# Kernel tuning notes

Measured on AMD Instinct MI355X. Metric: run time of the kernel, lower is better.

The kernel has to match this reference:

```python
import jax, jax.numpy as jnp
import numpy as np

B, T, D, K = 64, 4096, 90, 32
LOG2PI = 1.8378770664093453


def setup_inputs() -> dict:
    key = jax.random.key(0)
    k1, k2, k3, k4, k5 = jax.random.split(key, 5)
    X = jax.random.normal(k1, (B, T, D), dtype=jnp.float32)
    state_priors = jax.random.uniform(k2, (K,), dtype=jnp.float32)
    transition_matrix = jax.random.uniform(k3, (K, K), dtype=jnp.float32)
    mu = jax.random.normal(k4, (K, D), dtype=jnp.float32) * 0.5
    log_var = jax.random.normal(k5, (K, D), dtype=jnp.float32) * 0.1
    return {"X": X, "state_priors": state_priors,
            "transition_matrix": transition_matrix, "mu": mu, "log_var": log_var}


def _emission_logprobs(X, mu, log_var):
    # Diagonal-Gaussian log density per state: (B,T,K)
    # expand (x-mu)^2*inv_var to avoid materializing a (B,T,K,D) tensor
    inv_var = jnp.exp(-log_var)                                   # (K,D)
    quad = (jnp.einsum('btd,kd->btk', X * X, inv_var)
            - 2.0 * jnp.einsum('btd,kd->btk', X, mu * inv_var)
            + jnp.sum(mu * mu * inv_var, axis=-1))                # (B,T,K)
    return -0.5 * (quad + jnp.sum(log_var, axis=-1) + D * LOG2PI)


def reference(X, state_priors, transition_matrix, mu, log_var):
    log_A = jax.nn.log_softmax(transition_matrix, axis=1)   # (K,K)
    log_pi = jax.nn.log_softmax(state_priors, axis=0)       # (K,)
    em = _emission_logprobs(X, mu, log_var)                 # (B,T,K)

    log_alpha0 = log_pi + em[:, 0, :]                       # (B,K)

    def step(log_alpha, e_t):
        # log_alpha: (B,K), e_t: (B,K)
        la = e_t + jax.nn.logsumexp(log_alpha[:, :, None] + log_A[None], axis=1)
        return la, None

    em_rest = jnp.swapaxes(em[:, 1:, :], 0, 1)              # (T-1,B,K)
    log_alpha_T, _ = jax.lax.scan(step, log_alpha0, em_rest)
    # sum over subjects of logsumexp over states at final timestep
    return jnp.sum(jax.nn.logsumexp(log_alpha_T, axis=-1))
```

## Files before the change

### kernel.cpp

```cpp
#include <hip/hip_runtime.h>
#include <stdint.h>

#define B_ 64
#define T_ 4096
#define D_ 90
#define K_ 32
#define CH_ 32
#define F_  128
#define NB_ 2048

typedef float f32x16 __attribute__((ext_vector_type(16)));
typedef __bf16 bf16x8 __attribute__((ext_vector_type(8)));

#define WS_A     0
#define WS_PI    1024
#define WS_C0    1056
#define WS_WF    1088
#define WS_EACC  4160
#define WS_MS    12352
#define WS_E0    20544
#define WS_Q2    22080

#define LDS_WREG(w) ((w) * 1280)
#define LDS_WF      5120
#define LDS_TOT     11264

__device__ __forceinline__ int perm_r(int r) {
  int t2 = (r >> 2) & 3;
  return r + ((t2 == 1) ? 4 : (t2 == 2) ? -4 : 0);
}
__device__ __forceinline__ uint32_t pk2(float hi, float lo) {
  return __builtin_amdgcn_perm(__float_as_uint(hi), __float_as_uint(lo), 0x07060302u);
}
__device__ __forceinline__ uint32_t rnd_pk(float hi, float lo) {
  uint32_t uh = __float_as_uint(hi) + 0x8000u;
  uint32_t ul = __float_as_uint(lo) + 0x8000u;
  return __builtin_amdgcn_perm(uh, ul, 0x07060302u);
}
__device__ __forceinline__ float bf2f(ushort u) {
  return __uint_as_float(((uint32_t)u) << 16);
}
__device__ __forceinline__ bf16x8 mkbf(uint32_t a, uint32_t b, uint32_t c, uint32_t d) {
  union { uint32_t u[4]; bf16x8 v; } x;
  x.u[0] = a; x.u[1] = b; x.u[2] = c; x.u[3] = d;
  return x.v;
}

__global__ __launch_bounds__(1024) void prep_kernel(
    const float* __restrict__ priors, const float* __restrict__ trans,
    const float* __restrict__ mu, const float* __restrict__ lv,
    float* __restrict__ ws) {
  int tid = threadIdx.x;
  {
    float v = trans[tid];
    float m = v;
    #pragma unroll
    for (int mk = 16; mk; mk >>= 1) m = fmaxf(m, __shfl_xor(m, mk));
    float e = expf(v - m);
    float s = e;
    #pragma unroll
    for (int mk = 16; mk; mk >>= 1) s += __shfl_xor(s, mk);
    ws[WS_A + tid] = e / s;
  }
  if (tid < 32) {
    float v = priors[tid];
    float m = v;
    #pragma unroll
    for (int mk = 16; mk; mk >>= 1) m = fmaxf(m, __shfl_xor(m, mk));
    float e = expf(v - m);
    float s = e;
    #pragma unroll
    for (int mk = 16; mk; mk >>= 1) s += __shfl_xor(s, mk);
    ws[WS_PI + tid] = e / s;
  }
  for (int i = tid; i < 6144; i += 1024) {
    int j = i & 7, l = (i >> 3) & 63, cm = i >> 9;
    int c = cm >> 1, mat = cm & 1;
    int h = l >> 5, nn = l & 31;
    int d = 16 * c + 8 * h + j;
    float v = 0.0f;
    if (d < D_) {
      float ivd = expf(-lv[nn * D_ + d]);
      v = (mat == 0) ? -0.5f * ivd : mu[nn * D_ + d] * ivd;
    }
    ((ushort*)(ws + WS_WF))[i] = (ushort)((__float_as_uint(v) + 0x8000u) >> 16);
  }
  if (tid < 32) {
    float s = 0.0f;
    for (int d = 0; d < D_; ++d) {
      float l  = lv[tid * D_ + d];
      float iv = expf(-l);
      float m_ = mu[tid * D_ + d];
      s += m_ * m_ * iv + l;
    }
    ws[WS_C0 + tid] = -0.5f * (s + (float)D_ * 1.8378770664093453f);
  }
}

__global__ __launch_bounds__(256, 6) void fused_kernel(const float* __restrict__ X,
                                                       float* __restrict__ ws,
                                                       float* __restrict__ out) {
  __shared__ __align__(16) ushort sh[LDS_TOT];
  __shared__ float msb[4];
  __shared__ int   peb[4];
  int tid = threadIdx.x;
  int l = tid & 63, w = tid >> 6;
  int n = l & 31, h = l >> 5;
  int tB = blockIdx.x << 7;
  int t0 = tB + (w << 5);
  int b  = t0 >> 12;
  if (blockIdx.x == 0 && tid == 0) *out = 0.0f;

  {
    const uint4* wfp = (const uint4*)((const ushort*)(ws + WS_WF));
    uint4* wfl = (uint4*)(sh + LDS_WF);
    #pragma unroll
    for (int k = 0; k < 3; ++k) wfl[tid + (k << 8)] = wfp[tid + (k << 8)];
  }
  float c0 = ws[WS_C0 + n];

  int srow = l >> 1, sp = l & 1;
  const float* xg = X + (size_t)(t0 + srow) * D_ + 8 * sp;
  ushort* xbuf = sh + LDS_WREG(w);
  float2 va[4];
  auto xload = [&](int c) {
    #pragma unroll
    for (int s = 0; s < 4; ++s) {
      int d = 16 * c + 8 * sp + 2 * s;
      if (d < D_) va[s] = *(const float2*)(xg + 16 * c + 2 * s);
      else { va[s].x = 0.0f; va[s].y = 0.0f; }
    }
  };
  auto xwrite = [&]() {
    uint4 pkv;
    pkv.x = rnd_pk(va[0].y, va[0].x);
    pkv.y = rnd_pk(va[1].y, va[1].x);
    pkv.z = rnd_pk(va[2].y, va[2].x);
    pkv.w = rnd_pk(va[3].y, va[3].x);
    *(uint4*)(xbuf + srow * 24 + 8 * sp) = pkv;
  };
  xload(0);
  xwrite();
  xload(1);
  __syncthreads();

  const ushort* wfl = sh + LDS_WF;
  f32x16 acc;
  #pragma unroll
  for (int r = 0; r < 16; ++r) acc[r] = 0.0f;
  #pragma unroll
  for (int c = 0; c < 6; ++c) {
    union { uint4 u; bf16x8 v; } xb;
    xb.u = *(const uint4*)(xbuf + n * 24 + 8 * h);
    float x[8];
    #pragma unroll
    for (int j = 0; j < 8; ++j) {
      uint32_t uu = ((const uint32_t*)&xb.u)[j >> 1];
      x[j] = bf2f((j & 1) ? (ushort)(uu >> 16) : (ushort)(uu & 0xFFFF));
    }
    union { uint32_t u[4]; bf16x8 v; } x2b;
    #pragma unroll
    for (int r = 0; r < 4; ++r)
      x2b.u[r] = rnd_pk(x[2*r+1] * x[2*r+1], x[2*r] * x[2*r]);
    union { uint4 u; bf16x8 v; } w1, w2;
    w2.u = *(const uint4*)(wfl + (2 * c)     * 512 + l * 8);
    w1.u = *(const uint4*)(wfl + (2 * c + 1) * 512 + l * 8);
    acc = __builtin_amdgcn_mfma_f32_32x32x16_bf16(xb.v,  w1.v, acc, 0, 0, 0);
    acc = __builtin_amdgcn_mfma_f32_32x32x16_bf16(x2b.v, w2.v, acc, 0, 0, 0);
    if (c < 5) {
      xwrite();
      if (c < 4) xload(c + 2);
    }
  }
  float em[16], mrow[16];
  #pragma unroll
  for (int r = 0; r < 16; ++r) {
    float v = acc[r] + c0;
    em[r] = v;
    float m = v;
    #pragma unroll
    for (int mk = 1; mk <= 16; mk <<= 1) m = fmaxf(m, __shfl_xor(m, mk));
    mrow[r] = m;
  }
  ushort* Ew = sh + LDS_WREG(w);
  #pragma unroll
  for (int q = 0; q < 4; ++q) {
    float e0 = exp2f((em[4*q]   - mrow[4*q])   * 1.44269504088896f);
    float e1 = exp2f((em[4*q+1] - mrow[4*q+1]) * 1.44269504088896f);
    float e2 = exp2f((em[4*q+2] - mrow[4*q+2]) * 1.44269504088896f);
    float e3 = exp2f((em[4*q+3] - mrow[4*q+3]) * 1.44269504088896f);
    uint2 d;
    d.x = rnd_pk(e1, e0);
    d.y = rnd_pk(e3, e2);
    *(uint2*)(Ew + n * 40 + 8 * q + 4 * h) = d;
    if (q == 0 && h == 0 && (t0 & (T_ - 1)) == 0)
      ((ushort*)(ws + WS_E0))[b * K_ + n] = (ushort)(d.x & 0xFFFF);
  }
  float msum = 0.0f;
  #pragma unroll
  for (int r = 0; r < 16; ++r) msum += mrow[r];
  msum += __shfl_xor(msum, 32);
  if (l == 0) msb[w] = msum;

  int col = perm_r(n);
  const float* A = ws + WS_A;
  float astat[16];
  #pragma unroll
  for (int j = 0; j < 8; ++j) {
    astat[j]     = A[(8 * h + j) * K_ + col];
    astat[8 + j] = A[(16 + 8 * h + j) * K_ + col];
  }
  uint32_t q[8];
  #pragma unroll
  for (int r = 0; r < 4; ++r) {
    int s0 = 8 * h + 2 * r;
    uint32_t lo = (s0 == n)     ? 0x3F80u : 0u;
    uint32_t hi = (s0 + 1 == n) ? 0x3F80u : 0u;
    q[r] = lo | (hi << 16);
    int s2 = s0 + 16;
    lo = (s2 == n)     ? 0x3F80u : 0u;
    hi = (s2 + 1 == n) ? 0x3F80u : 0u;
    q[4 + r] = lo | (hi << 16);
  }
  int eacc = 0;
  const f32x16 z = {0.f,0.f,0.f,0.f,0.f,0.f,0.f,0.f,0.f,0.f,0.f,0.f,0.f,0.f,0.f,0.f};
  #pragma unroll
  for (int r = 0; r < 16; ++r) acc[r] = 0.0f;

  auto step = [&](float e0) {
    uint32_t au[8];
    #pragma unroll
    for (int r = 0; r < 4; ++r) {
      au[r]     = pk2(astat[2 * r + 1] * e0, astat[2 * r] * e0);
      au[4 + r] = pk2(astat[8 + 2 * r + 1] * e0, astat[8 + 2 * r] * e0);
    }
    bf16x8 alo = mkbf(au[0], au[1], au[2], au[3]);
    bf16x8 ahi = mkbf(au[4], au[5], au[6], au[7]);
    bf16x8 qlo = mkbf(q[0], q[1], q[2], q[3]);
    bf16x8 qhi = mkbf(q[4], q[5], q[6], q[7]);
    acc = __builtin_amdgcn_mfma_f32_32x32x16_bf16(alo, qlo, z, 0, 0, 0);
    acc = __builtin_amdgcn_mfma_f32_32x32x16_bf16(ahi, qhi, acc, 0, 0, 0);
    #pragma unroll
    for (int r = 0; r < 4; ++r) {
      q[r]     = pk2(acc[2 * r + 1], acc[2 * r]);
      q[4 + r] = pk2(acc[8 + 2 * r + 1], acc[8 + 2 * r]);
    }
  };
  auto lmul = [&](uint4 lo, uint4 hi) {
    bf16x8 alo = mkbf(lo.x, lo.y, lo.z, lo.w);
    bf16x8 ahi = mkbf(hi.x, hi.y, hi.z, hi.w);
    bf16x8 qlo = mkbf(q[0], q[1], q[2], q[3]);
    bf16x8 qhi = mkbf(q[4], q[5], q[6], q[7]);
    acc = __builtin_amdgcn_mfma_f32_32x32x16_bf16(alo, qlo, z, 0, 0, 0);
    acc = __builtin_amdgcn_mfma_f32_32x32x16_bf16(ahi, qhi, acc, 0, 0, 0);
    #pragma unroll
    for (int r = 0; r < 4; ++r) {
      q[r]     = pk2(acc[2 * r + 1], acc[2 * r]);
      q[4 + r] = pk2(acc[8 + 2 * r + 1], acc[8 + 2 * r]);
    }
  };
  auto renorm = [&]() {
    float m = acc[0];
    #pragma unroll
    for (int r = 1; r < 16; ++r) m = fmaxf(m, acc[r]);
    #pragma unroll
    for (int mk = 1; mk <= 32; mk <<= 1) m = fmaxf(m, __shfl_xor(m, mk));
    int ex;
    frexpf(m, &ex);
    float sc = ldexpf(1.0f, -ex);
    eacc += ex;
    #pragma unroll
    for (int r = 0; r < 16; ++r) acc[r] *= sc;
    #pragma unroll
    for (int r = 0; r < 4; ++r) {
      q[r]     = pk2(acc[2 * r + 1], acc[2 * r]);
      q[4 + r] = pk2(acc[8 + 2 * r + 1], acc[8 + 2 * r]);
    }
  };

  const ushort* Eb = sh + LDS_WREG(w) + col * 40;
  int g0 = 0;
  if ((t0 & (T_ - 1)) == 0) {
    uint4 ev = *(const uint4*)(Eb);
    #pragma unroll
    for (int j = 1; j < 8; ++j) {
      uint32_t u = ((const uint32_t*)&ev)[j >> 1];
      step(bf2f((j & 1) ? (ushort)(u >> 16) : (ushort)(u & 0xFFFF)));
    }
    renorm();
    g0 = 1;
  }
  for (int g = g0; g < CH_ / 8; ++g) {
    uint4 ev = *(const uint4*)(Eb + 8 * g);
    #pragma unroll
    for (int j = 0; j < 8; ++j) {
      uint32_t u = ((const uint32_t*)&ev)[j >> 1];
      step(bf2f((j & 1) ? (ushort)(u >> 16) : (ushort)(u & 0xFFFF)));
    }
    renorm();
  }

  ushort* Qw = sh + LDS_WREG(w);
  #pragma unroll
  for (int r = 0; r < 16; ++r) {
    int m_ = (r & 3) + 8 * (r >> 2) + 4 * h;
    Qw[perm_r(m_) * 40 + n] = (ushort)(__float_as_uint(acc[r]) >> 16);
  }
  if (l == 0) peb[w] = eacc;
  __syncthreads();
  if (w != 0) return;

  #pragma unroll
  for (int r = 0; r < 4; ++r) {
    int s0 = 8 * h + 2 * r;
    uint32_t lo = (s0 == n)     ? 0x3F80u : 0u;
    uint32_t hi = (s0 + 1 == n) ? 0x3F80u : 0u;
    q[r] = lo | (hi << 16);
    int s2 = s0 + 16;
    lo = (s2 == n)     ? 0x3F80u : 0u;
    hi = (s2 + 1 == n) ? 0x3F80u : 0u;
    q[4 + r] = lo | (hi << 16);
  }
  eacc = peb[0] + peb[1] + peb[2] + peb[3];
  float msm = msb[0] + msb[1] + msb[2] + msb[3];
  #pragma unroll
  for (int p = 0; p < 4; ++p) {
    const ushort* base = sh + LDS_WREG(p) + col * 40;
    uint4 lo = *(const uint4*)(base + 8 * h);
    uint4 hi = *(const uint4*)(base + 16 + 8 * h);
    lmul(lo, hi);
  }
  renorm();
  ushort* Qo = (ushort*)(ws + WS_Q2) + (size_t)blockIdx.x * (K_ * K_);
  #pragma unroll
  for (int r = 0; r < 16; ++r) {
    int m_ = (r & 3) + 8 * (r >> 2) + 4 * h;
    Qo[perm_r(m_) * K_ + n] = (ushort)(__float_as_uint(acc[r]) >> 16);
  }
  if (l == 0) {
    ((int*)ws)[WS_EACC + blockIdx.x] = eacc;
    ws[WS_MS + blockIdx.x] = msm;
  }
}

__global__ __launch_bounds__(256) void combine_kernel(float* __restrict__ ws,
                                                      float* __restrict__ out) {
  __shared__ __align__(16) ushort pm[4][1280];
  __shared__ int pe[4];
  int tid = threadIdx.x;
  int l = tid & 63, w = tid >> 6;
  int h = l >> 5, n = l & 31;
  int b = blockIdx.x;
  int row = perm_r(n);
  int eacc;
  {
    const int* ea = ((const int*)ws) + WS_EACC + b * 32 + w * 8;
    int v = (l < 8) ? ea[l] : 0;
    #pragma unroll
    for (int mk = 1; mk <= 4; mk <<= 1) v += __shfl_xor(v, mk);
    eacc = __shfl(v, 0);
  }
  uint32_t q[8];
  #pragma unroll
  for (int r = 0; r < 4; ++r) {
    int s0 = 8 * h + 2 * r;
    uint32_t lo = (s0 == n)     ? 0x3F80u : 0u;
    uint32_t hi = (s0 + 1 == n) ? 0x3F80u : 0u;
    q[r] = lo | (hi << 16);
    int s2 = s0 + 16;
    lo = (s2 == n)     ? 0x3F80u : 0u;
    hi = (s2 + 1 == n) ? 0x3F80u : 0u;
    q[4 + r] = lo | (hi << 16);
  }
  f32x16 acc;
  #pragma unroll
  for (int r = 0; r < 16; ++r) acc[r] = 0.0f;
  const f32x16 z = {0.f,0.f,0.f,0.f,0.f,0.f,0.f,0.f,0.f,0.f,0.f,0.f,0.f,0.f,0.f,0.f};

  auto lmul = [&](uint4 lo, uint4 hi) {
    bf16x8 alo = mkbf(lo.x, lo.y, lo.z, lo.w);
    bf16x8 ahi = mkbf(hi.x, hi.y, hi.z, hi.w);
    bf16x8 qlo = mkbf(q[0], q[1], q[2], q[3]);
    bf16x8 qhi = mkbf(q[4], q[5], q[6], q[7]);
    acc = __builtin_amdgcn_mfma_f32_32x32x16_bf16(alo, qlo, z, 0, 0, 0);
    acc = __builtin_amdgcn_mfma_f32_32x32x16_bf16(ahi, qhi, acc, 0, 0, 0);
    #pragma unroll
    for (int r = 0; r < 4; ++r) {
      q[r]     = pk2(acc[2 * r + 1], acc[2 * r]);
      q[4 + r] = pk2(acc[8 + 2 * r + 1], acc[8 + 2 * r]);
    }
  };
  auto renorm = [&]() {
    float m = acc[0];
    #pragma unroll
    for (int r = 1; r < 16; ++r) m = fmaxf(m, acc[r]);
    #pragma unroll
    for (int mk = 1; mk <= 32; mk <<= 1) m = fmaxf(m, __shfl_xor(m, mk));
    int ex;
    frexpf(m, &ex);
    float sc = ldexpf(1.0f, -ex);
    eacc += ex;
    #pragma unroll
    for (int r = 0; r < 16; ++r) acc[r] *= sc;
    #pragma unroll
    for (int r = 0; r < 4; ++r) {
      q[r]     = pk2(acc[2 * r + 1], acc[2 * r]);
      q[4 + r] = pk2(acc[8 + 2 * r + 1], acc[8 + 2 * r]);
    }
  };

  const ushort* Qb = (const ushort*)(ws + WS_Q2) + (size_t)(b * 32 + w * 8) * (K_ * K_);
  #pragma unroll
  for (int p = 0; p < 8; ++p) {
    const ushort* Mc = Qb + (size_t)p * (K_ * K_) + row * K_;
    uint4 lo = *(const uint4*)(Mc + 8 * h);
    uint4 hi = *(const uint4*)(Mc + 16 + 8 * h);
    lmul(lo, hi);
    if ((p & 3) == 3) renorm();
  }
  #pragma unroll
  for (int r = 0; r < 16; ++r) {
    int m_ = (r & 3) + 8 * (r >> 2) + 4 * h;
    pm[w][perm_r(m_) * 40 + n] = (ushort)(__float_as_uint(acc[r]) >> 16);
  }
  if (l == 0) pe[w] = eacc;
  __syncthreads();
  if (w != 0) return;

  float alpha0 = ws[WS_PI + n] * bf2f(((const ushort*)(ws + WS_E0))[b * K_ + n]);
  float msm;
  {
    float v = (l < 32) ? ws[WS_MS + b * 32 + l] : 0.0f;
    #pragma unroll
    for (int mk = 1; mk <= 32; mk <<= 1) v += __shfl_xor(v, mk);
    msm = v;
  }
  #pragma unroll
  for (int r = 0; r < 4; ++r) {
    int s0 = 8 * h + 2 * r;
    uint32_t lo = (s0 == n)     ? 0x3F80u : 0u;
    uint32_t hi = (s0 + 1 == n) ? 0x3F80u : 0u;
    q[r] = lo | (hi << 16);
    int s2 = s0 + 16;
    lo = (s2 == n)     ? 0x3F80u : 0u;
    hi = (s2 + 1 == n) ? 0x3F80u : 0u;
    q[4 + r] = lo | (hi << 16);
  }
  #pragma unroll
  for (int r = 0; r < 16; ++r) acc[r] = 0.0f;
  int et = pe[0] + pe[1] + pe[2] + pe[3];
  #pragma unroll
  for (int p = 0; p < 4; ++p) {
    const ushort* base = pm[p] + row * 40;
    uint4 lo = *(const uint4*)(base + 8 * h);
    uint4 hi = *(const uint4*)(base + 16 + 8 * h);
    lmul(lo, hi);
  }
  float part = 0.0f;
  #pragma unroll
  for (int r = 0; r < 16; ++r) part += acc[r];
  part *= alpha0;
  #pragma unroll
  for (int mk = 1; mk <= 32; mk <<= 1) part += __shfl_xor(part, mk);
  if (l == 0) {
    float res = logf(part) + (float)et * 0.69314718055994531f + msm;
    atomicAdd(out, res);
  }
}

extern "C" void kernel_launch(void* const* d_in, const int* in_sizes, int n_in,
                              void* d_out, int out_size, void* d_ws, size_t ws_size,
                              hipStream_t stream) {
  (void)in_sizes; (void)n_in; (void)out_size; (void)ws_size;
  const float* X      = (const float*)d_in[0];
  const float* priors = (const float*)d_in[1];
  const float* trans  = (const float*)d_in[2];
  const float* mu     = (const float*)d_in[3];
  const float* lv     = (const float*)d_in[4];
  float* ws  = (float*)d_ws;
  float* out = (float*)d_out;
  prep_kernel<<<1, 1024, 0, stream>>>(priors, trans, mu, lv, ws);
  fused_kernel<<<NB_, 256, 0, stream>>>(X, ws, out);
  combine_kernel<<<B_, 256, 0, stream>>>(ws, out);
}
```

Measured before the change: 174.6 us.

## Give each wave two interleaved 32-step chunks to hide MFMA dependency latency

Each block now covers 256 timesteps, and each wave handles two 32-step chunks. The two chunks' transfer-matrix products run as independent chains that alternate, so their MFMA latencies overlap and fill stalls in the serial recurrence. The block-level composition now multiplies 8 chunk matrices, and the grid shrinks to 1024 blocks, which halves the work in the combine kernel. In exchange LDS use and register pressure go up and launch bounds occupancy drops from 6 to 4 blocks per CU. A stray label also appears in the code.

```diff
diff --git a/kernel.cpp b/kernel.cpp
--- a/kernel.cpp
+++ b/kernel.cpp
@@ -6,8 +6,7 @@
 #define D_ 90
 #define K_ 32
 #define CH_ 32
-#define F_  128
-#define NB_ 2048
+#define NB_ 1024
 
 typedef float f32x16 __attribute__((ext_vector_type(16)));
 typedef __bf16 bf16x8 __attribute__((ext_vector_type(8)));
@@ -21,9 +20,9 @@
 #define WS_E0    20544
 #define WS_Q2    22080
 
-#define LDS_WREG(w) ((w) * 1280)
-#define LDS_WF      5120
-#define LDS_TOT     11264
+#define LDS_CREG(c) ((c) * 1280)
+#define LDS_WF      10240
+#define LDS_TOT     16384
 
 __device__ __forceinline__ int perm_r(int r) {
   int t2 = (r >> 2) & 3;
@@ -97,7 +96,7 @@
   }
 }
 
-__global__ __launch_bounds__(256, 6) void fused_kernel(const float* __restrict__ X,
+__global__ __launch_bounds__(256, 4) void fused_kernel(const float* __restrict__ X,
                                                        float* __restrict__ ws,
                                                        float* __restrict__ out) {
   __shared__ __align__(16) ushort sh[LDS_TOT];
@@ -106,8 +105,8 @@
   int tid = threadIdx.x;
   int l = tid & 63, w = tid >> 6;
   int n = l & 31, h = l >> 5;
-  int tB = blockIdx.x << 7;
-  int t0 = tB + (w << 5);
+  int tB = blockIdx.x << 8;
+  int t0 = tB + (w << 6);
   int b  = t0 >> 12;
   if (blockIdx.x == 0 && tid == 0) *out = 0.0f;
 
@@ -120,10 +119,9 @@
   float c0 = ws[WS_C0 + n];
 
   int srow = l >> 1, sp = l & 1;
-  const float* xg = X + (size_t)(t0 + srow) * D_ + 8 * sp;
-  ushort* xbuf = sh + LDS_WREG(w);
+  const float* xg0 = X + (size_t)(t0 + srow) * D_ + 8 * sp;
   float2 va[4];
-  auto xload = [&](int c) {
+  auto xload = [&](const float* xg, int c) {
     #pragma unroll
     for (int s = 0; s < 4; ++s) {
       int d = 16 * c + 8 * sp + 2 * s;
@@ -131,74 +129,80 @@
       else { va[s].x = 0.0f; va[s].y = 0.0f; }
     }
   };
-  auto xwrite = [&]() {
+  auto xwrite = [&](ushort* xb) {
     uint4 pkv;
     pkv.x = rnd_pk(va[0].y, va[0].x);
     pkv.y = rnd_pk(va[1].y, va[1].x);
     pkv.z = rnd_pk(va[2].y, va[2].x);
     pkv.w = rnd_pk(va[3].y, va[3].x);
-    *(uint4*)(xbuf + srow * 24 + 8 * sp) = pkv;
-  };
-  xload(0);
-  xwrite();
-  xload(1);
+    *(uint4*)(xb + srow * 24 + 8 * sp) = pkv;
+  };
+  xload(xg0, 0);
+  xwrite(sh + LDS_CREG(2 * w));
+  xload(xg0, 1);
   __syncthreads();
 
   const ushort* wfl = sh + LDS_WF;
-  f32x16 acc;
-  #pragma unroll
-  for (int r = 0; r < 16; ++r) acc[r] = 0.0f;
-  #pragma unroll
-  for (int c = 0; c < 6; ++c) {
-    union { uint4 u; bf16x8 v; } xb;
-    xb.u = *(const uint4*)(xbuf + n * 24 + 8 * h);
-    float x[8];
-    #pragma unroll
-    for (int j = 0; j < 8; ++j) {
-      uint32_t uu = ((const uint32_t*)&xb.u)[j >> 1];
-      x[j] = bf2f((j & 1) ? (ushort)(uu >> 16) : (ushort)(uu & 0xFFFF));
-    }
-    union { uint32_t u[4]; bf16x8 v; } x2b;
-    #pragma unroll
-    for (int r = 0; r < 4; ++r)
-      x2b.u[r] = rnd_pk(x[2*r+1] * x[2*r+1], x[2*r] * x[2*r]);
-    union { uint4 u; bf16x8 v; } w1, w2;
-    w2.u = *(const uint4*)(wfl + (2 * c)     * 512 + l * 8);
-    w1.u = *(const uint4*)(wfl + (2 * c + 1) * 512 + l * 8);
-    acc = __builtin_amdgcn_mfma_f32_32x32x16_bf16(xb.v,  w1.v, acc, 0, 0, 0);
-    acc = __builtin_amdgcn_mfma_f32_32x32x16_bf16(x2b.v, w2.v, acc, 0, 0, 0);
-    if (c < 5) {
-      xwrite();
-      if (c < 4) xload(c + 2);
-    }
-  }
-  float em[16], mrow[16];
-  #pragma unroll
-  for (int r = 0; r < 16; ++r) {
-    float v = acc[r] + c0;
-    em[r] = v;
-    float m = v;
-    #pragma unroll
-    for (int mk = 1; mk <= 16; mk <<= 1) m = fmaxf(m, __shfl_xor(m, mk));
-    mrow[r] = m;
-  }
-  ushort* Ew = sh + LDS_WREG(w);
-  #pragma unroll
-  for (int q = 0; q < 4; ++q) {
-    float e0 = exp2f((em[4*q]   - mrow[4*q])   * 1.44269504088896f);
-    float e1 = exp2f((em[4*q+1] - mrow[4*q+1]) * 1.44269504088896f);
-    float e2 = exp2f((em[4*q+2] - mrow[4*q+2]) * 1.44269504088896f);
-    float e3 = exp2f((em[4*q+3] - mrow[4*q+3]) * 1.44269504088896f);
-    uint2 d;
-    d.x = rnd_pk(e1, e0);
-    d.y = rnd_pk(e3, e2);
-    *(uint2*)(Ew + n * 40 + 8 * q + 4 * h) = d;
-    if (q == 0 && h == 0 && (t0 & (T_ - 1)) == 0)
-      ((ushort*)(ws + WS_E0))[b * K_ + n] = (ushort)(d.x & 0xFFFF);
-  }
+  bool firstA = ((t0 & (T_ - 1)) == 0);
   float msum = 0.0f;
   #pragma unroll
-  for (int r = 0; r < 16; ++r) msum += mrow[r];
+  for (int i = 0; i < 2; ++i) {
+    const float* xg = xg0 + (size_t)(32 * i) * D_;
+    ushort* xbuf = sh + LDS_CREG(2 * w + i);
+    if (i == 1) { xload(xg, 0); xwrite(xbuf); xload(xg, 1); }
+    f32x16 acc;
+    #pragma unroll
+    for (int r = 0; r < 16; ++r) acc[r] = 0.0f;
+    #pragma unroll
+    for (int c = 0; c < 6; ++c) {
+      union { uint4 u; bf16x8 v; } xb;
+      xb.u = *(const uint4*)(xbuf + n * 24 + 8 * h);
+      float x[8];
+      #pragma unroll
+      for (int j = 0; j < 8; ++j) {
+        uint32_t uu = ((const uint32_t*)&xb.u)[j >> 1];
+        x[j] = bf2f((j & 1) ? (ushort)(uu >> 16) : (ushort)(uu & 0xFFFF));
+      }
+      union { uint32_t u[4]; bf16x8 v; } x2b;
+      #pragma unroll
+      for (int r = 0; r < 4; ++r)
+        x2b.u[r] = rnd_pk(x[2*r+1] * x[2*r+1], x[2*r] * x[2*r]);
+      union { uint4 u; bf16x8 v; } w1, w2;
+      w2.u = *(const uint4*)(wfl + (2 * c)     * 512 + l * 8);
+      w1.u = *(const uint4*)(wfl + (2 * c + 1) * 512 + l * 8);
+      acc = __builtin_amdgcn_mfma_f32_32x32x16_bf16(xb.v,  w1.v, acc, 0, 0, 0);
+      acc = __builtin_amdgcn_mfma_f32_32x32x16_bf16(x2b.v, w2.v, acc, 0, 0, 0);
+      if (c < 5) {
+        xwrite(xbuf);
+        if (c < 4) xload(xg, c + 2);
+      }
+    }
+    float em[16], mrow[16];
+    #pragma unroll
+    for (int r = 0; r < 16; ++r) {
+      float v = acc[r] + c0;
+      em[r] = v;
+      float m = v;
+      #pragma unroll
+      for (int mk = 1; mk <= 16; mk <<= 1) m = fmaxf(m, __shfl_xor(m, mk));
+      mrow[r] = m;
+    }
+    #pragma unroll
+    for (int q = 0; q < 4; ++q) {
+      float e0 = exp2f((em[4*q]   - mrow[4*q])   * 1.44269504088896f);
+      float e1 = exp2f((em[4*q+1] - mrow[4*q+1]) * 1.44269504088896f);
+      float e2 = exp2f((em[4*q+2] - mrow[4*q+2]) * 1.44269504088896f);
+      float e3 = exp2f((em[4*q+3] - mrow[4*q+3]) * 1.44269504088896f);
+      uint2 d;
+      d.x = rnd_pk(e1, e0);
+      d.y = rnd_pk(e3, e2);
+      *(uint2*)(xbuf + n * 40 + 8 * q + 4 * h) = d;
+      if (i == 0 && q == 0 && h == 0 && firstA)
+        ((ushort*)(ws + WS_E0))[b * K_ + n] = (ushort)(d.x & 0xFFFF);
+    }
+    #pragma unroll
+    for (int r = 0; r < 16; ++r) msum += mrow[r];
+  }
   msum += __shfl_xor(msum, 32);
   if (l == 0) msb[w] = msum;
 
@@ -210,24 +214,25 @@
     astat[j]     = A[(8 * h + j) * K_ + col];
     astat[8 + j] = A[(16 + 8 * h + j) * K_ + col];
   }
-  uint32_t q[8];
+  int eacc = 0;
+  const f32x16 z = {0.f,0.f,0.f,0.f,0.f,0.f,0.f,0.f,0.f,0.f,0.f,0.f,0.f,0.f,0.f,0.f};
+  f32x16 accA, accB;
+  uint32_t qA[8], qB[8];
+  #pragma unroll
+  for (int r = 0; r < 16; ++r) { accA[r] = 0.0f; accB[r] = 0.0f; }
   #pragma unroll
   for (int r = 0; r < 4; ++r) {
     int s0 = 8 * h + 2 * r;
     uint32_t lo = (s0 == n)     ? 0x3F80u : 0u;
     uint32_t hi = (s0 + 1 == n) ? 0x3F80u : 0u;
-    q[r] = lo | (hi << 16);
+    qA[r] = lo | (hi << 16);  qB[r] = qA[r];
     int s2 = s0 + 16;
     lo = (s2 == n)     ? 0x3F80u : 0u;
     hi = (s2 + 1 == n) ? 0x3F80u : 0u;
-    q[4 + r] = lo | (hi << 16);
-  }
-  int eacc = 0;
-  const f32x16 z = {0.f,0.f,0.f,0.f,0.f,0.f,0.f,0.f,0.f,0.f,0.f,0.f,0.f,0.f,0.f,0.f};
-  #pragma unroll
-  for (int r = 0; r < 16; ++r) acc[r] = 0.0f;
-
-  auto step = [&](float e0) {
+    qA[4 + r] = lo | (hi << 16);  qB[4 + r] = qA[4 + r];
+  }
+
+  auto stepc = [&](f32x16& acc, uint32_t (&q)[8], float e0) {
     uint32_t au[8];
     #pragma unroll
     for (int r = 0; r < 4; ++r) {
@@ -246,20 +251,7 @@
       q[4 + r] = pk2(acc[8 + 2 * r + 1], acc[8 + 2 * r]);
     }
   };
-  auto lmul = [&](uint4 lo, uint4 hi) {
-    bf16x8 alo = mkbf(lo.x, lo.y, lo.z, lo.w);
-    bf16x8 ahi = mkbf(hi.x, hi.y, hi.z, hi.w);
-    bf16x8 qlo = mkbf(q[0], q[1], q[2], q[3]);
-    bf16x8 qhi = mkbf(q[4], q[5], q[6], q[7]);
-    acc = __builtin_amdgcn_mfma_f32_32x32x16_bf16(alo, qlo, z, 0, 0, 0);
-    acc = __builtin_amdgcn_mfma_f32_32x32x16_bf16(ahi, qhi, acc, 0, 0, 0);
-    #pragma unroll
-    for (int r = 0; r < 4; ++r) {
-      q[r]     = pk2(acc[2 * r + 1], acc[2 * r]);
-      q[4 + r] = pk2(acc[8 + 2 * r + 1], acc[8 + 2 * r]);
-    }
-  };
-  auto renorm = [&]() {
+  auto renormc = [&](f32x16& acc, uint32_t (&q)[8]) {
     float m = acc[0];
     #pragma unroll
     for (int r = 1; r < 16; ++r) m = fmaxf(m, acc[r]);
@@ -278,33 +270,34 @@
     }
   };
 
-  const ushort* Eb = sh + LDS_WREG(w) + col * 40;
-  int g0 = 0;
-  if ((t0 & (T_ - 1)) == 0) {
-    uint4 ev = *(const uint4*)(Eb);
-    #pragma unroll
-    for (int j = 1; j < 8; ++j) {
-      uint32_t u = ((const uint32_t*)&ev)[j >> 1];
-      step(bf2f((j & 1) ? (ushort)(u >> 16) : (ushort)(u & 0xFFFF)));
-    }
-    renorm();
-    g0 = 1;
-  }
-  for (int g = g0; g < CH_ / 8; ++g) {
-    uint4 ev = *(const uint4*)(Eb + 8 * g);
+  const ushort* EbA = sh + LDS_CREG(2 * w)     + col * 40;
+  const ushort* EbB = sh + LDS_CREG(2 * w + 1) + col * 40;
+  #pragma unroll
+  for (int g = 0; g < 4; ++g) {
+    uint4 evA = *(const uint4*)(EbA + 8 * g);
+    uint4 evB = *(const uint4*)(EbB + 8 * g);
     #pragma unroll
     for (int j = 0; j < 8; ++j) {
-      uint32_t u = ((const uint32_t*)&ev)[j >> 1];
-      step(bf2f((j & 1) ? (ushort)(u >> 16) : (ushort)(u & 0xFFFF)));
-    }
-    renorm();
-  }
-
-  ushort* Qw = sh + LDS_WREG(w);
+      uint32_t uA = ((const uint32_t*)&evA)[j >> 1];
+      uint32_t uB = ((const uint32_t*)&evB)[j >> 1];
+      float eA = bf2f((j & 1) ? (ushort)(uA >> 16) : (ushort)(uA & 0xFFFF));
+      float eB = bf2f((j & 1) ? (ushort)(uB >> 16) : (ushort)(uB & 0xFFFF));
+      if (g == 0 && j == 0) {
+        if (!firstA) stepc(accA, qA, eA);
+      } else {
+        stepc(accA, qA, eA);
+      }
+      stepc(accB, qB, eB);
+    }
+    renormc(accA, qA);
+    renormc(accB, qB);
+  }
+
   #pragma unroll
   for (int r = 0; r < 16; ++r) {
-    int m_ = (r & 3) + 8 * (r >> 2) + 4 * h;
-    Qw[perm_r(m_) * 40 + n] = (ushort)(__float_as_uint(acc[r]) >> 16);
+    int m_ = perm_r((r & 3) + 8 * (r >> 2) + 4 * h) * 40 + n;
+    (sh + LDS_CREG(2 * w))[m_]     = (ushort)(__float_as_uint(accA[r]) >> 16);
+    (sh + LDS_CREG(2 * w + 1))[m_] = (ushort)(__float_as_uint(accB[r]) >> 16);
   }
   if (l == 0) peb[w] = eacc;
   __syncthreads();
@@ -315,27 +308,41 @@
     int s0 = 8 * h + 2 * r;
     uint32_t lo = (s0 == n)     ? 0x3F80u : 0u;
     uint32_t hi = (s0 + 1 == n) ? 0x3F80u : 0u;
-    q[r] = lo | (hi << 16);
+    qA[r] = lo | (hi << 16);
     int s2 = s0 + 16;
     lo = (s2 == n)     ? 0x3F80u : 0u;
     hi = (s2 + 1 == n) ? 0x3F80u : 0u;
-    q[4 + r] = lo | (hi << 16);
+    qA[4 + r] = lo | (hi << 16);
   }
   eacc = peb[0] + peb[1] + peb[2] + peb[3];
   float msm = msb[0] + msb[1] + msb[2] + msb[3];
   #pragma unroll
-  for (int p = 0; p < 4; ++p) {
-    const ushort* base = sh + LDS_WREG(p) + col * 40;
+  for (int r = 0; r < 16; ++r) accA[r] = 0.0f;
+  #pragma unroll
+  for (int p = 0; p < 8; ++p) {
+    const ushort* base = sh + LDS_CREG(p) + col * 40;
     uint4 lo = *(const uint4*)(base + 8 * h);
     uint4 hi = *(const uint4*)(base + 16 + 8 * h);
-    lmul(lo, hi);
-  }
-  renorm();
+    stepcompose:;
+    bf16x8 alo = mkbf(lo.x, lo.y, lo.z, lo.w);
+    bf16x8 ahi = mkbf(hi.x, hi.y, hi.z, hi.w);
+    bf16x8 qlo = mkbf(qA[0], qA[1], qA[2], qA[3]);
+    bf16x8 qhi = mkbf(qA[4], qA[5], qA[6], qA[7]);
+    accA = __builtin_amdgcn_mfma_f32_32x32x16_bf16(alo, qlo, z, 0, 0, 0);
+    accA = __builtin_amdgcn_mfma_f32_32x32x16_bf16(ahi, qhi, accA, 0, 0, 0);
+    #pragma unroll
+    for (int r = 0; r < 4; ++r) {
+      qA[r]     = pk2(accA[2 * r + 1], accA[2 * r]);
+      qA[4 + r] = pk2(accA[8 + 2 * r + 1], accA[8 + 2 * r]);
+    }
+    if (p == 3) renormc(accA, qA);
+  }
+  renormc(accA, qA);
   ushort* Qo = (ushort*)(ws + WS_Q2) + (size_t)blockIdx.x * (K_ * K_);
   #pragma unroll
   for (int r = 0; r < 16; ++r) {
     int m_ = (r & 3) + 8 * (r >> 2) + 4 * h;
-    Qo[perm_r(m_) * K_ + n] = (ushort)(__float_as_uint(acc[r]) >> 16);
+    Qo[perm_r(m_) * K_ + n] = (ushort)(__float_as_uint(accA[r]) >> 16);
   }
   if (l == 0) {
     ((int*)ws)[WS_EACC + blockIdx.x] = eacc;
@@ -354,10 +361,10 @@
   int row = perm_r(n);
   int eacc;
   {
-    const int* ea = ((const int*)ws) + WS_EACC + b * 32 + w * 8;
-    int v = (l < 8) ? ea[l] : 0;
-    #pragma unroll
-    for (int mk = 1; mk <= 4; mk <<= 1) v += __shfl_xor(v, mk);
+    const int* ea = ((const int*)ws) + WS_EACC + b * 16 + w * 4;
+    int v = (l < 4) ? ea[l] : 0;
+    #pragma unroll
+    for (int mk = 1; mk <= 2; mk <<= 1) v += __shfl_xor(v, mk);
     eacc = __shfl(v, 0);
   }
   uint32_t q[8];
@@ -409,15 +416,15 @@
     }
   };
 
-  const ushort* Qb = (const ushort*)(ws + WS_Q2) + (size_t)(b * 32 + w * 8) * (K_ * K_);
-  #pragma unroll
-  for (int p = 0; p < 8; ++p) {
+  const ushort* Qb = (const ushort*)(ws + WS_Q2) + (size_t)(b * 16 + w * 4) * (K_ * K_);
+  #pragma unroll
+  for (int p = 0; p < 4; ++p) {
     const ushort* Mc = Qb + (size_t)p * (K_ * K_) + row * K_;
     uint4 lo = *(const uint4*)(Mc + 8 * h);
     uint4 hi = *(const uint4*)(Mc + 16 + 8 * h);
     lmul(lo, hi);
-    if ((p & 3) == 3) renorm();
-  }
+  }
+  renorm();
   #pragma unroll
   for (int r = 0; r < 16; ++r) {
     int m_ = (r & 3) + 8 * (r >> 2) + 4 * h;
@@ -430,7 +437,7 @@
   float alpha0 = ws[WS_PI + n] * bf2f(((const ushort*)(ws + WS_E0))[b * K_ + n]);
   float msm;
   {
-    float v = (l < 32) ? ws[WS_MS + b * 32 + l] : 0.0f;
+    float v = (l < 16) ? ws[WS_MS + b * 16 + l] : 0.0f;
     #pragma unroll
     for (int mk = 1; mk <= 32; mk <<= 1) v += __shfl_xor(v, mk);
     msm = v;
```

After: 183.8 us. 1.05x slower.

## Move per-block chunk matrix reduction from fused kernel into combine kernel

Applied to the files above, without the earlier changes.

Each wave in the fused kernel now writes its own 32-step transfer matrix, exponent and max-sum straight to global workspace. The old intra-block barrier, where wave 0 multiplied four matrices while the others sat idle, is gone. The combine kernel now chains 32 matrices per wave instead of 8, with a 4-deep register prefetch of the global loads and a renormalisation every 8 products. LDS padding shrinks and the launch bound rises to 8 blocks per CU to allow higher occupancy. The trade-off is more global traffic and a longer serial MFMA chain in the combine kernel.

```diff
diff --git a/kernel.cpp b/kernel.cpp
--- a/kernel.cpp
+++ b/kernel.cpp
@@ -19,11 +19,11 @@
 #define WS_EACC  4160
 #define WS_MS    12352
 #define WS_E0    20544
-#define WS_Q2    22080
-
-#define LDS_WREG(w) ((w) * 1280)
-#define LDS_WF      5120
-#define LDS_TOT     11264
+#define WS_Q     22080
+
+#define LDS_WREG(w) ((w) * 1024)
+#define LDS_WF      4096
+#define LDS_TOT     10240
 
 __device__ __forceinline__ int perm_r(int r) {
   int t2 = (r >> 2) & 3;
@@ -97,18 +97,17 @@
   }
 }
 
-__global__ __launch_bounds__(256, 6) void fused_kernel(const float* __restrict__ X,
+__global__ __launch_bounds__(256, 8) void fused_kernel(const float* __restrict__ X,
                                                        float* __restrict__ ws,
                                                        float* __restrict__ out) {
   __shared__ __align__(16) ushort sh[LDS_TOT];
-  __shared__ float msb[4];
-  __shared__ int   peb[4];
   int tid = threadIdx.x;
   int l = tid & 63, w = tid >> 6;
   int n = l & 31, h = l >> 5;
   int tB = blockIdx.x << 7;
   int t0 = tB + (w << 5);
   int b  = t0 >> 12;
+  int bc = t0 >> 5;
   if (blockIdx.x == 0 && tid == 0) *out = 0.0f;
 
   {
@@ -172,35 +171,30 @@
       if (c < 4) xload(c + 2);
     }
   }
-  float em[16], mrow[16];
-  #pragma unroll
-  for (int r = 0; r < 16; ++r) {
-    float v = acc[r] + c0;
-    em[r] = v;
-    float m = v;
-    #pragma unroll
-    for (int mk = 1; mk <= 16; mk <<= 1) m = fmaxf(m, __shfl_xor(m, mk));
-    mrow[r] = m;
-  }
-  ushort* Ew = sh + LDS_WREG(w);
-  #pragma unroll
-  for (int q = 0; q < 4; ++q) {
-    float e0 = exp2f((em[4*q]   - mrow[4*q])   * 1.44269504088896f);
-    float e1 = exp2f((em[4*q+1] - mrow[4*q+1]) * 1.44269504088896f);
-    float e2 = exp2f((em[4*q+2] - mrow[4*q+2]) * 1.44269504088896f);
-    float e3 = exp2f((em[4*q+3] - mrow[4*q+3]) * 1.44269504088896f);
+  bool first = ((t0 & (T_ - 1)) == 0);
+  ushort* Ew = xbuf;
+  float msum = 0.0f;
+  #pragma unroll
+  for (int qq = 0; qq < 4; ++qq) {
+    float e0[4];
+    #pragma unroll
+    for (int i = 0; i < 4; ++i) {
+      float v = acc[4 * qq + i] + c0;
+      float m = v;
+      #pragma unroll
+      for (int mk = 1; mk <= 16; mk <<= 1) m = fmaxf(m, __shfl_xor(m, mk));
+      e0[i] = exp2f((v - m) * 1.44269504088896f);
+      msum += m;
+    }
     uint2 d;
-    d.x = rnd_pk(e1, e0);
-    d.y = rnd_pk(e3, e2);
-    *(uint2*)(Ew + n * 40 + 8 * q + 4 * h) = d;
-    if (q == 0 && h == 0 && (t0 & (T_ - 1)) == 0)
+    d.x = rnd_pk(e0[1], e0[0]);
+    d.y = rnd_pk(e0[3], e0[2]);
+    *(uint2*)(Ew + n * 32 + 8 * qq + 4 * h) = d;
+    if (qq == 0 && h == 0 && first)
       ((ushort*)(ws + WS_E0))[b * K_ + n] = (ushort)(d.x & 0xFFFF);
   }
-  float msum = 0.0f;
-  #pragma unroll
-  for (int r = 0; r < 16; ++r) msum += mrow[r];
   msum += __shfl_xor(msum, 32);
-  if (l == 0) msb[w] = msum;
+  if (l == 0) ws[WS_MS + bc] = msum;
 
   int col = perm_r(n);
   const float* A = ws + WS_A;
@@ -246,19 +240,6 @@
       q[4 + r] = pk2(acc[8 + 2 * r + 1], acc[8 + 2 * r]);
     }
   };
-  auto lmul = [&](uint4 lo, uint4 hi) {
-    bf16x8 alo = mkbf(lo.x, lo.y, lo.z, lo.w);
-    bf16x8 ahi = mkbf(hi.x, hi.y, hi.z, hi.w);
-    bf16x8 qlo = mkbf(q[0], q[1], q[2], q[3]);
-    bf16x8 qhi = mkbf(q[4], q[5], q[6], q[7]);
-    acc = __builtin_amdgcn_mfma_f32_32x32x16_bf16(alo, qlo, z, 0, 0, 0);
-    acc = __builtin_amdgcn_mfma_f32_32x32x16_bf16(ahi, qhi, acc, 0, 0, 0);
-    #pragma unroll
-    for (int r = 0; r < 4; ++r) {
-      q[r]     = pk2(acc[2 * r + 1], acc[2 * r]);
-      q[4 + r] = pk2(acc[8 + 2 * r + 1], acc[8 + 2 * r]);
-    }
-  };
   auto renorm = [&]() {
     float m = acc[0];
     #pragma unroll
@@ -278,9 +259,9 @@
     }
   };
 
-  const ushort* Eb = sh + LDS_WREG(w) + col * 40;
+  const ushort* Eb = sh + LDS_WREG(w) + col * 32;
   int g0 = 0;
-  if ((t0 & (T_ - 1)) == 0) {
+  if (first) {
     uint4 ev = *(const uint4*)(Eb);
     #pragma unroll
     for (int j = 1; j < 8; ++j) {
@@ -300,47 +281,13 @@
     renorm();
   }
 
-  ushort* Qw = sh + LDS_WREG(w);
-  #pragma unroll
-  for (int r = 0; r < 16; ++r) {
-    int m_ = (r & 3) + 8 * (r >> 2) + 4 * h;
-    Qw[perm_r(m_) * 40 + n] = (ushort)(__float_as_uint(acc[r]) >> 16);
-  }
-  if (l == 0) peb[w] = eacc;
-  __syncthreads();
-  if (w != 0) return;
-
-  #pragma unroll
-  for (int r = 0; r < 4; ++r) {
-    int s0 = 8 * h + 2 * r;
-    uint32_t lo = (s0 == n)     ? 0x3F80u : 0u;
-    uint32_t hi = (s0 + 1 == n) ? 0x3F80u : 0u;
-    q[r] = lo | (hi << 16);
-    int s2 = s0 + 16;
-    lo = (s2 == n)     ? 0x3F80u : 0u;
-    hi = (s2 + 1 == n) ? 0x3F80u : 0u;
-    q[4 + r] = lo | (hi << 16);
-  }
-  eacc = peb[0] + peb[1] + peb[2] + peb[3];
-  float msm = msb[0] + msb[1] + msb[2] + msb[3];
-  #pragma unroll
-  for (int p = 0; p < 4; ++p) {
-    const ushort* base = sh + LDS_WREG(p) + col * 40;
-    uint4 lo = *(const uint4*)(base + 8 * h);
-    uint4 hi = *(const uint4*)(base + 16 + 8 * h);
-    lmul(lo, hi);
-  }
-  renorm();
-  ushort* Qo = (ushort*)(ws + WS_Q2) + (size_t)blockIdx.x * (K_ * K_);
+  ushort* Qo = (ushort*)(ws + WS_Q) + (size_t)bc * (K_ * K_);
   #pragma unroll
   for (int r = 0; r < 16; ++r) {
     int m_ = (r & 3) + 8 * (r >> 2) + 4 * h;
     Qo[perm_r(m_) * K_ + n] = (ushort)(__float_as_uint(acc[r]) >> 16);
   }
-  if (l == 0) {
-    ((int*)ws)[WS_EACC + blockIdx.x] = eacc;
-    ws[WS_MS + blockIdx.x] = msm;
-  }
+  if (l == 0) ((int*)ws)[WS_EACC + bc] = eacc;
 }
 
 __global__ __launch_bounds__(256) void combine_kernel(float* __restrict__ ws,
@@ -354,10 +301,10 @@
   int row = perm_r(n);
   int eacc;
   {
-    const int* ea = ((const int*)ws) + WS_EACC + b * 32 + w * 8;
-    int v = (l < 8) ? ea[l] : 0;
-    #pragma unroll
-    for (int mk = 1; mk <= 4; mk <<= 1) v += __shfl_xor(v, mk);
+    const int* ea = ((const int*)ws) + WS_EACC + b * F_ + w * 32;
+    int v = (l < 32) ? ea[l] : 0;
+    #pragma unroll
+    for (int mk = 1; mk <= 16; mk <<= 1) v += __shfl_xor(v, mk);
     eacc = __shfl(v, 0);
   }
   uint32_t q[8];
@@ -409,14 +356,23 @@
     }
   };
 
-  const ushort* Qb = (const ushort*)(ws + WS_Q2) + (size_t)(b * 32 + w * 8) * (K_ * K_);
-  #pragma unroll
-  for (int p = 0; p < 8; ++p) {
+  const ushort* Qb = (const ushort*)(ws + WS_Q) + (size_t)(b * F_ + w * 32) * (K_ * K_);
+  uint4 rlo[4], rhi[4];
+  #pragma unroll
+  for (int p = 0; p < 4; ++p) {
     const ushort* Mc = Qb + (size_t)p * (K_ * K_) + row * K_;
-    uint4 lo = *(const uint4*)(Mc + 8 * h);
-    uint4 hi = *(const uint4*)(Mc + 16 + 8 * h);
-    lmul(lo, hi);
-    if ((p & 3) == 3) renorm();
+    rlo[p] = *(const uint4*)(Mc + 8 * h);
+    rhi[p] = *(const uint4*)(Mc + 16 + 8 * h);
+  }
+  #pragma unroll
+  for (int c = 0; c < 32; ++c) {
+    lmul(rlo[c & 3], rhi[c & 3]);
+    if (c + 4 < 32) {
+      const ushort* Mc = Qb + (size_t)(c + 4) * (K_ * K_) + row * K_;
+      rlo[c & 3] = *(const uint4*)(Mc + 8 * h);
+      rhi[c & 3] = *(const uint4*)(Mc + 16 + 8 * h);
+    }
+    if ((c & 7) == 7) renorm();
   }
   #pragma unroll
   for (int r = 0; r < 16; ++r) {
@@ -430,7 +386,7 @@
   float alpha0 = ws[WS_PI + n] * bf2f(((const ushort*)(ws + WS_E0))[b * K_ + n]);
   float msm;
   {
-    float v = (l < 32) ? ws[WS_MS + b * 32 + l] : 0.0f;
+    float v = ws[WS_MS + b * F_ + l] + ws[WS_MS + b * F_ + 64 + l];
     #pragma unroll
     for (int mk = 1; mk <= 32; mk <<= 1) v += __shfl_xor(v, mk);
     msm = v;
```

After: 182.0 us. 4.3% more time.

## Double fused-kernel block size to 8 waves, halving blocks and combine partials

Applied to the files above, without the earlier changes.

Each block of the fused kernel now has 8 waves covering 256 timesteps instead of 4 waves covering 128. Each block therefore reduces 8 chunk matrices in-block, and the combine kernel has only 16 partial products per sequence to multiply instead of 32. The emission softmax epilogue is restructured to reuse the X staging buffer and use fewer live registers, and the C0 prep is parallelised across 1024 threads with a shuffle reduction. The larger blocks reduce global partial traffic and combine work, but make the serial in-block product chain longer and may lower occupancy under the new launch bounds.

```diff
diff --git a/kernel.cpp b/kernel.cpp
--- a/kernel.cpp
+++ b/kernel.cpp
@@ -6,8 +6,7 @@
 #define D_ 90
 #define K_ 32
 #define CH_ 32
-#define F_  128
-#define NB_ 2048
+#define NB_ 1024
 
 typedef float f32x16 __attribute__((ext_vector_type(16)));
 typedef __bf16 bf16x8 __attribute__((ext_vector_type(8)));
@@ -22,8 +21,8 @@
 #define WS_Q2    22080
 
 #define LDS_WREG(w) ((w) * 1280)
-#define LDS_WF      5120
-#define LDS_TOT     11264
+#define LDS_WF      10240
+#define LDS_TOT     16384
 
 __device__ __forceinline__ int perm_r(int r) {
   int t2 = (r >> 2) & 3;
@@ -85,28 +84,31 @@
     }
     ((ushort*)(ws + WS_WF))[i] = (ushort)((__float_as_uint(v) + 0x8000u) >> 16);
   }
-  if (tid < 32) {
+  {
+    int nn = tid >> 5, j = tid & 31;
     float s = 0.0f;
-    for (int d = 0; d < D_; ++d) {
-      float l  = lv[tid * D_ + d];
-      float iv = expf(-l);
-      float m_ = mu[tid * D_ + d];
-      s += m_ * m_ * iv + l;
-    }
-    ws[WS_C0 + tid] = -0.5f * (s + (float)D_ * 1.8378770664093453f);
-  }
-}
-
-__global__ __launch_bounds__(256, 6) void fused_kernel(const float* __restrict__ X,
+    for (int d = j; d < D_; d += 32) {
+      float lvv = lv[nn * D_ + d];
+      float iv  = expf(-lvv);
+      float m_  = mu[nn * D_ + d];
+      s += m_ * m_ * iv + lvv;
+    }
+    #pragma unroll
+    for (int mk = 16; mk; mk >>= 1) s += __shfl_xor(s, mk);
+    if (j == 0) ws[WS_C0 + nn] = -0.5f * (s + (float)D_ * 1.8378770664093453f);
+  }
+}
+
+__global__ __launch_bounds__(512, 8) void fused_kernel(const float* __restrict__ X,
                                                        float* __restrict__ ws,
                                                        float* __restrict__ out) {
   __shared__ __align__(16) ushort sh[LDS_TOT];
-  __shared__ float msb[4];
-  __shared__ int   peb[4];
+  __shared__ float msb[8];
+  __shared__ int   peb[8];
   int tid = threadIdx.x;
   int l = tid & 63, w = tid >> 6;
   int n = l & 31, h = l >> 5;
-  int tB = blockIdx.x << 7;
+  int tB = blockIdx.x << 8;
   int t0 = tB + (w << 5);
   int b  = t0 >> 12;
   if (blockIdx.x == 0 && tid == 0) *out = 0.0f;
@@ -115,7 +117,10 @@
     const uint4* wfp = (const uint4*)((const ushort*)(ws + WS_WF));
     uint4* wfl = (uint4*)(sh + LDS_WF);
     #pragma unroll
-    for (int k = 0; k < 3; ++k) wfl[tid + (k << 8)] = wfp[tid + (k << 8)];
+    for (int k = 0; k < 2; ++k) {
+      int i = tid + (k << 9);
+      if (i < 768) wfl[i] = wfp[i];
+    }
   }
   float c0 = ws[WS_C0 + n];
 
@@ -172,33 +177,27 @@
       if (c < 4) xload(c + 2);
     }
   }
-  float em[16], mrow[16];
-  #pragma unroll
-  for (int r = 0; r < 16; ++r) {
-    float v = acc[r] + c0;
-    em[r] = v;
-    float m = v;
-    #pragma unroll
-    for (int mk = 1; mk <= 16; mk <<= 1) m = fmaxf(m, __shfl_xor(m, mk));
-    mrow[r] = m;
-  }
-  ushort* Ew = sh + LDS_WREG(w);
-  #pragma unroll
-  for (int q = 0; q < 4; ++q) {
-    float e0 = exp2f((em[4*q]   - mrow[4*q])   * 1.44269504088896f);
-    float e1 = exp2f((em[4*q+1] - mrow[4*q+1]) * 1.44269504088896f);
-    float e2 = exp2f((em[4*q+2] - mrow[4*q+2]) * 1.44269504088896f);
-    float e3 = exp2f((em[4*q+3] - mrow[4*q+3]) * 1.44269504088896f);
+  bool first = ((t0 & (T_ - 1)) == 0);
+  float msum = 0.0f;
+  #pragma unroll
+  for (int qq = 0; qq < 4; ++qq) {
+    float e0[4];
+    #pragma unroll
+    for (int i = 0; i < 4; ++i) {
+      float v = acc[4 * qq + i] + c0;
+      float m = v;
+      #pragma unroll
+      for (int mk = 1; mk <= 16; mk <<= 1) m = fmaxf(m, __shfl_xor(m, mk));
+      e0[i] = exp2f((v - m) * 1.44269504088896f);
+      msum += m;
+    }
     uint2 d;
-    d.x = rnd_pk(e1, e0);
-    d.y = rnd_pk(e3, e2);
-    *(uint2*)(Ew + n * 40 + 8 * q + 4 * h) = d;
-    if (q == 0 && h == 0 && (t0 & (T_ - 1)) == 0)
+    d.x = rnd_pk(e0[1], e0[0]);
+    d.y = rnd_pk(e0[3], e0[2]);
+    *(uint2*)(xbuf + n * 40 + 8 * qq + 4 * h) = d;
+    if (qq == 0 && h == 0 && first)
       ((ushort*)(ws + WS_E0))[b * K_ + n] = (ushort)(d.x & 0xFFFF);
   }
-  float msum = 0.0f;
-  #pragma unroll
-  for (int r = 0; r < 16; ++r) msum += mrow[r];
   msum += __shfl_xor(msum, 32);
   if (l == 0) msb[w] = msum;
 
@@ -280,7 +279,7 @@
 
   const ushort* Eb = sh + LDS_WREG(w) + col * 40;
   int g0 = 0;
-  if ((t0 & (T_ - 1)) == 0) {
+  if (first) {
     uint4 ev = *(const uint4*)(Eb);
     #pragma unroll
     for (int j = 1; j < 8; ++j) {
@@ -321,14 +320,19 @@
     hi = (s2 + 1 == n) ? 0x3F80u : 0u;
     q[4 + r] = lo | (hi << 16);
   }
-  eacc = peb[0] + peb[1] + peb[2] + peb[3];
-  float msm = msb[0] + msb[1] + msb[2] + msb[3];
-  #pragma unroll
-  for (int p = 0; p < 4; ++p) {
+  eacc = 0;
+  float msm = 0.0f;
+  #pragma unroll
+  for (int p = 0; p < 8; ++p) { eacc += peb[p]; msm += msb[p]; }
+  #pragma unroll
+  for (int r = 0; r < 16; ++r) acc[r] = 0.0f;
+  #pragma unroll
+  for (int p = 0; p < 8; ++p) {
     const ushort* base = sh + LDS_WREG(p) + col * 40;
     uint4 lo = *(const uint4*)(base + 8 * h);
     uint4 hi = *(const uint4*)(base + 16 + 8 * h);
     lmul(lo, hi);
+    if (p == 3) renorm();
   }
   renorm();
   ushort* Qo = (ushort*)(ws + WS_Q2) + (size_t)blockIdx.x * (K_ * K_);
@@ -354,10 +358,10 @@
   int row = perm_r(n);
   int eacc;
   {
-    const int* ea = ((const int*)ws) + WS_EACC + b * 32 + w * 8;
-    int v = (l < 8) ? ea[l] : 0;
-    #pragma unroll
-    for (int mk = 1; mk <= 4; mk <<= 1) v += __shfl_xor(v, mk);
+    const int* ea = ((const int*)ws) + WS_EACC + b * 16 + w * 4;
+    int v = (l < 4) ? ea[l] : 0;
+    #pragma unroll
+    for (int mk = 1; mk <= 2; mk <<= 1) v += __shfl_xor(v, mk);
     eacc = __shfl(v, 0);
   }
   uint32_t q[8];
@@ -409,15 +413,15 @@
     }
   };
 
-  const ushort* Qb = (const ushort*)(ws + WS_Q2) + (size_t)(b * 32 + w * 8) * (K_ * K_);
-  #pragma unroll
-  for (int p = 0; p < 8; ++p) {
+  const ushort* Qb = (const ushort*)(ws + WS_Q2) + (size_t)(b * 16 + w * 4) * (K_ * K_);
+  #pragma unroll
+  for (int p = 0; p < 4; ++p) {
     const ushort* Mc = Qb + (size_t)p * (K_ * K_) + row * K_;
     uint4 lo = *(const uint4*)(Mc + 8 * h);
     uint4 hi = *(const uint4*)(Mc + 16 + 8 * h);
     lmul(lo, hi);
-    if ((p & 3) == 3) renorm();
-  }
+  }
+  renorm();
   #pragma unroll
   for (int r = 0; r < 16; ++r) {
     int m_ = (r & 3) + 8 * (r >> 2) + 4 * h;
@@ -430,7 +434,7 @@
   float alpha0 = ws[WS_PI + n] * bf2f(((const ushort*)(ws + WS_E0))[b * K_ + n]);
   float msm;
   {
-    float v = (l < 32) ? ws[WS_MS + b * 32 + l] : 0.0f;
+    float v = (l < 16) ? ws[WS_MS + b * 16 + l] : 0.0f;
     #pragma unroll
     for (int mk = 1; mk <= 32; mk <<= 1) v += __shfl_xor(v, mk);
     msm = v;
@@ -480,6 +484,6 @@
   float* ws  = (float*)d_ws;
   float* out = (float*)d_out;
   prep_kernel<<<1, 1024, 0, stream>>>(priors, trans, mu, lv, ws);
-  fused_kernel<<<NB_, 256, 0, stream>>>(X, ws, out);
+  fused_kernel<<<NB_, 512, 0, stream>>>(X, ws, out);
   combine_kernel<<<B_, 256, 0, stream>>>(ws, out);
 }
```

Measured after the change: 178.5 us. 1.02x slower.
